# Optimization experiments

Measured on AMD Instinct MI355X. Metric: run time of the kernel, lower is better.

Reference implementation:

```python
import jax, jax.numpy as jnp
import numpy as np

B, L, D, H, FF, NS = 4, 1024, 1024, 16, 4096, 64
HD = D // H
EPS = 1e-5


def layer_norm(x, g, b):
    mu = jnp.mean(x, axis=-1, keepdims=True)
    var = jnp.mean(jnp.square(x - mu), axis=-1, keepdims=True)
    return (x - mu) * jax.lax.rsqrt(var + EPS) * g + b


def mha(xq, xkv, wqkv, bqkv, wo, bo, bias=None):
    # torch nn.MultiheadAttention with packed in_proj: rows [0:D]=Q, [D:2D]=K, [2D:3D]=V
    Bq, Lq, Dm = xq.shape
    q = (xq @ wqkv[:Dm].T + bqkv[:Dm]).reshape(Bq, Lq, H, HD).transpose(0, 2, 1, 3)
    k = (xkv @ wqkv[Dm:2 * Dm].T + bqkv[Dm:2 * Dm]).reshape(Bq, -1, H, HD).transpose(0, 2, 1, 3)
    v = (xkv @ wqkv[2 * Dm:].T + bqkv[2 * Dm:]).reshape(Bq, -1, H, HD).transpose(0, 2, 1, 3)
    scores = jnp.einsum('bhqd,bhkd->bhqk', q, k) / np.sqrt(HD).astype(np.float32)
    if bias is not None:
        scores = scores + bias.reshape(Bq, H, Lq, -1)
    attn = jax.nn.softmax(scores, axis=-1)
    out = jnp.einsum('bhqk,bhkd->bhqd', attn, v).transpose(0, 2, 1, 3).reshape(Bq, Lq, Dm)
    return out @ wo.T + bo


def setup_inputs() -> dict:
    key = jax.random.key(0)
    ks = jax.random.split(key, 16)
    w = lambda k, shape: jax.random.normal(k, shape, jnp.float32) * 0.02
    return {
        'x': jax.random.normal(ks[0], (B, L, D), jnp.float32),
        'alibi_bias': jax.random.normal(ks[1], (B * H, L, L), jnp.float32) * 0.1,
        'species_emb': jax.random.normal(ks[2], (B, NS, D), jnp.float32),
        'norm1_g': jnp.ones(D), 'norm1_b': jnp.zeros(D),
        'sa_wqkv': w(ks[3], (3 * D, D)), 'sa_bqkv': jnp.zeros(3 * D),
        'sa_wo': w(ks[4], (D, D)), 'sa_bo': jnp.zeros(D),
        'ca_nq_g': jnp.ones(D), 'ca_nq_b': jnp.zeros(D),
        'ca_nkv_g': jnp.ones(D), 'ca_nkv_b': jnp.zeros(D),
        'ca_wqkv': w(ks[5], (3 * D, D)), 'ca_bqkv': jnp.zeros(3 * D),
        'ca_wo': w(ks[6], (D, D)), 'ca_bo': jnp.zeros(D),
        'gate_param': jnp.float32(0.1),
        'ffn_g': jnp.ones(D), 'ffn_b': jnp.zeros(D),
        'ffn_w1': w(ks[7], (2 * FF, D)), 'ffn_b1': jnp.zeros(2 * FF),
        'ffn_w2': w(ks[8], (D, FF)), 'ffn_b2': jnp.zeros(D),
    }


def reference(x, alibi_bias, species_emb,
              norm1_g, norm1_b, sa_wqkv, sa_bqkv, sa_wo, sa_bo,
              ca_nq_g, ca_nq_b, ca_nkv_g, ca_nkv_b, ca_wqkv, ca_bqkv, ca_wo, ca_bo,
              gate_param, ffn_g, ffn_b, ffn_w1, ffn_b1, ffn_w2, ffn_b2):
    # 1) pre-norm self-attention with ALiBi additive bias
    h = layer_norm(x, norm1_g, norm1_b)
    h = mha(h, h, sa_wqkv, sa_bqkv, sa_wo, sa_bo, bias=alibi_bias)
    x = x + h  # dropout is identity in eval mode
    # 2) gated cross-attention with species embeddings
    q = layer_norm(x, ca_nq_g, ca_nq_b)
    kv = layer_norm(species_emb, ca_nkv_g, ca_nkv_b)
    cross = mha(q, kv, ca_wqkv, ca_bqkv, ca_wo, ca_bo)
    x = x + jax.nn.sigmoid(gate_param) * cross
    # 3) GEGLU feed-forward
    f = layer_norm(x, ffn_g, ffn_b) @ ffn_w1.T + ffn_b1
    val, gate = f[..., :FF], f[..., FF:]
    f = (val * jax.nn.gelu(gate, approximate=False)) @ ffn_w2.T + ffn_b2
    return x + f
```

## Files before the change

### kernel.cpp

```cpp
#include <hip/hip_runtime.h>
#include <hip/hip_bf16.h>
#include <cstdint>

#define DEVI __device__ __forceinline__

typedef __attribute__((ext_vector_type(8))) short  short8;
typedef __attribute__((ext_vector_type(8))) __bf16 bf16x8;
typedef __attribute__((ext_vector_type(4))) float  f32x4;

DEVI float bf2f(short s) {
    unsigned u = ((unsigned)(unsigned short)s) << 16;
    return __builtin_bit_cast(float, u);
}
DEVI short f2bf(float f) {
    unsigned u = __builtin_bit_cast(unsigned, f);
    u = u + 0x7FFF + ((u >> 16) & 1);
    return (short)(u >> 16);
}

__global__ __launch_bounds__(256) void cvt_bf16(const float* src, short* dst, long n) {
    const long i = ((long)blockIdx.x * 256 + threadIdx.x) * 8;
    const float4 a = *(const float4*)&src[i];
    const float4 b = *(const float4*)&src[i + 4];
    short8 o;
    o[0] = f2bf(a.x); o[1] = f2bf(a.y); o[2] = f2bf(a.z); o[3] = f2bf(a.w);
    o[4] = f2bf(b.x); o[5] = f2bf(b.y); o[6] = f2bf(b.z); o[7] = f2bf(b.w);
    *(short8*)&dst[i] = o;
}

struct GArgs {
    const short* A; long lda, sAb, sAh;
    const short* B; long ldb, sBb, sBh;
    short* C;       long ldc, sCb, sCh;
    const float* bias;
    const float* addm; long ldad, sDb, sDh;
    float* resid;
    float* outf;
    const float* gate;
    const float* addf;
    float scale;
    int K, nh;
};

template<int BM, int BN, int EPI>
__global__ __launch_bounds__(256) void gemm_bt(GArgs a) {
    constexpr int WM = BM / 2, WN = BN / 2, MI = WM / 16, NI = WN / 16;
    __shared__ __align__(16) short As[BM * 32];
    __shared__ __align__(16) short Bs[BN * 32];
    const int tid = threadIdx.x;
    const int wave = tid >> 6, lane = tid & 63;
    const int wm = (wave >> 1) * WM, wn = (wave & 1) * WN;
    const int q = lane >> 4, r = lane & 15;
    const int gx = gridDim.x, gy = gridDim.y;
    int flat = (int)(blockIdx.y * gx + blockIdx.x);
    { const int cp = (gx * gy) >> 3; flat = (flat & 7) * cp + (flat >> 3); }
    const int bx = flat % gx, by = flat / gx;
    const long bb = blockIdx.z / a.nh, hh = blockIdx.z % a.nh;
    const short* Ab = a.A + bb * a.sAb + hh * a.sAh + (long)by * BM * a.lda;
    const short* Bb = a.B + bb * a.sBb + hh * a.sBh + (long)bx * BN * a.ldb;
    const int trow = tid >> 2;
    const int tcol = (tid & 3) * 8;
    f32x4 acc[MI][NI] = {};

    for (int k0 = 0; k0 < a.K; k0 += 32) {
        __syncthreads();
#pragma unroll
        for (int i = 0; i < BM / 64; i++) {
            const short* g = Ab + (long)(i * 64 + trow) * a.lda + k0 + tcol;
            __builtin_amdgcn_global_load_lds(
                (const __attribute__((address_space(1))) void*)g,
                (__attribute__((address_space(3))) void*)&As[(i * 64 + trow) * 32 + tcol],
                16, 0, 0);
        }
#pragma unroll
        for (int i = 0; i < BN / 64; i++) {
            const short* g = Bb + (long)(i * 64 + trow) * a.ldb + k0 + tcol;
            __builtin_amdgcn_global_load_lds(
                (const __attribute__((address_space(1))) void*)g,
                (__attribute__((address_space(3))) void*)&Bs[(i * 64 + trow) * 32 + tcol],
                16, 0, 0);
        }
        asm volatile("s_waitcnt vmcnt(0)" ::: "memory");
        __syncthreads();
        bf16x8 av[MI], bv[NI];
#pragma unroll
        for (int mi = 0; mi < MI; mi++)
            av[mi] = __builtin_bit_cast(bf16x8, *(const short8*)&As[(wm + mi * 16 + r) * 32 + q * 8]);
#pragma unroll
        for (int ni = 0; ni < NI; ni++)
            bv[ni] = __builtin_bit_cast(bf16x8, *(const short8*)&Bs[(wn + ni * 16 + r) * 32 + q * 8]);
#pragma unroll
        for (int mi = 0; mi < MI; mi++)
#pragma unroll
            for (int ni = 0; ni < NI; ni++)
                acc[mi][ni] = __builtin_amdgcn_mfma_f32_16x16x32_bf16(av[mi], bv[ni], acc[mi][ni], 0, 0, 0);
    }

    const long m0 = (long)by * BM + wm;
    const long n0 = (long)bx * BN + wn;
    float gs = a.scale;
    if (EPI == 2 && a.gate) gs *= 1.f / (1.f + __expf(-(*a.gate)));
#pragma unroll
    for (int mi = 0; mi < MI; mi++)
#pragma unroll
        for (int ni = 0; ni < NI; ni++)
#pragma unroll
            for (int j = 0; j < 4; j++) {
                const long m = m0 + mi * 16 + q * 4 + j;
                const long n = n0 + ni * 16 + r;
                float v = acc[mi][ni][j];
                if constexpr (EPI == 0) {
                    if (a.bias) v += a.bias[n];
                    a.C[bb * a.sCb + hh * a.sCh + m * a.ldc + n] = f2bf(v);
                } else if constexpr (EPI == 1) {
                    v *= a.scale;
                    if (a.addm) v += a.addm[bb * a.sDb + hh * a.sDh + m * a.ldad + n];
                    a.C[bb * a.sCb + hh * a.sCh + m * a.ldc + n] = f2bf(v);
                } else if constexpr (EPI == 2) {
                    if (a.bias) v += a.bias[n];
                    const long idx = m * a.ldc + n;
                    const float base = a.addf ? a.addf[idx] : a.resid[idx];
                    a.resid[idx] = base + gs * v;
                } else {
                    if (a.bias) v += a.bias[n];
                    a.outf[m * a.ldc + n] = a.resid[m * a.ldc + n] + v;
                }
            }
}

struct GGArgs {
    const short* A; long lda;
    const short* Bv; const short* Bg; long ldb;
    short* C; long ldc;
    const float* b1;
    int K;
};
__global__ __launch_bounds__(256) void gemm_geglu(GGArgs a) {
    constexpr int BM = 128, BN = 64, WM = 64, WN = 32, MI = 4, NI = 2;
    __shared__ __align__(16) short As[BM * 32];
    __shared__ __align__(16) short Bs[BN * 32];
    __shared__ __align__(16) short Gs[BN * 32];
    const int tid = threadIdx.x;
    const int wave = tid >> 6, lane = tid & 63;
    const int wm = (wave >> 1) * WM, wn = (wave & 1) * WN;
    const int q = lane >> 4, r = lane & 15;
    const int gx = gridDim.x, gy = gridDim.y;
    int flat = (int)(blockIdx.y * gx + blockIdx.x);
    { const int cp = (gx * gy) >> 3; flat = (flat & 7) * cp + (flat >> 3); }
    const int bx = flat % gx, by = flat / gx;
    const short* Ab = a.A + (long)by * BM * a.lda;
    const short* Bb = a.Bv + (long)bx * BN * a.ldb;
    const short* Gb = a.Bg + (long)bx * BN * a.ldb;
    const int trow = tid >> 2, tcol = (tid & 3) * 8;
    f32x4 accv[MI][NI] = {}, accg[MI][NI] = {};

    for (int k0 = 0; k0 < a.K; k0 += 32) {
        __syncthreads();
#pragma unroll
        for (int i = 0; i < 2; i++) {
            const short* g = Ab + (long)(i * 64 + trow) * a.lda + k0 + tcol;
            __builtin_amdgcn_global_load_lds(
                (const __attribute__((address_space(1))) void*)g,
                (__attribute__((address_space(3))) void*)&As[(i * 64 + trow) * 32 + tcol],
                16, 0, 0);
        }
        {
            const short* g = Bb + (long)trow * a.ldb + k0 + tcol;
            __builtin_amdgcn_global_load_lds(
                (const __attribute__((address_space(1))) void*)g,
                (__attribute__((address_space(3))) void*)&Bs[trow * 32 + tcol], 16, 0, 0);
            const short* g2 = Gb + (long)trow * a.ldb + k0 + tcol;
            __builtin_amdgcn_global_load_lds(
                (const __attribute__((address_space(1))) void*)g2,
                (__attribute__((address_space(3))) void*)&Gs[trow * 32 + tcol], 16, 0, 0);
        }
        asm volatile("s_waitcnt vmcnt(0)" ::: "memory");
        __syncthreads();
        bf16x8 av[MI], bv[NI], gv[NI];
#pragma unroll
        for (int mi = 0; mi < MI; mi++)
            av[mi] = __builtin_bit_cast(bf16x8, *(const short8*)&As[(wm + mi * 16 + r) * 32 + q * 8]);
#pragma unroll
        for (int ni = 0; ni < NI; ni++) {
            bv[ni] = __builtin_bit_cast(bf16x8, *(const short8*)&Bs[(wn + ni * 16 + r) * 32 + q * 8]);
            gv[ni] = __builtin_bit_cast(bf16x8, *(const short8*)&Gs[(wn + ni * 16 + r) * 32 + q * 8]);
        }
#pragma unroll
        for (int mi = 0; mi < MI; mi++)
#pragma unroll
            for (int ni = 0; ni < NI; ni++) {
                accv[mi][ni] = __builtin_amdgcn_mfma_f32_16x16x32_bf16(av[mi], bv[ni], accv[mi][ni], 0, 0, 0);
                accg[mi][ni] = __builtin_amdgcn_mfma_f32_16x16x32_bf16(av[mi], gv[ni], accg[mi][ni], 0, 0, 0);
            }
    }

    const long m0 = (long)by * BM + wm;
    const long n0 = (long)bx * BN + wn;
#pragma unroll
    for (int mi = 0; mi < MI; mi++)
#pragma unroll
        for (int ni = 0; ni < NI; ni++)
#pragma unroll
            for (int j = 0; j < 4; j++) {
                const long m = m0 + mi * 16 + q * 4 + j;
                const long n = n0 + ni * 16 + r;
                const float v = accv[mi][ni][j] + a.b1[n];
                const float g = accg[mi][ni][j] + a.b1[4096 + n];
                const float ge = 0.5f * g * (1.f + erff(g * 0.7071067811865476f));
                a.C[m * a.ldc + n] = f2bf(v * ge);
            }
}

__global__ __launch_bounds__(256) void flash_sa(const short* qkv, const short* vt,
                                                const float* alibi, short* Obuf) {
    __shared__ __align__(16) short Qs[64 * 64], Ks[64 * 64], Vs[64 * 64], Ps[64 * 64];
    const int tid = threadIdx.x;
    const int wave = tid >> 6, lane = tid & 63, q = lane >> 4, r = lane & 15;
    int flat = (int)(blockIdx.y * 16 + blockIdx.x);
    flat = (flat & 7) * 128 + (flat >> 3);
    const int qt = flat & 15, bh = flat >> 4, b = bh >> 4, h = bh & 15;
    const long qrow0 = (long)b * 1024 + qt * 64;
    const int rw = tid >> 3, sp = tid & 7;

#pragma unroll
    for (int i = 0; i < 2; i++) {
        const int row = i * 32 + rw;
        const int c8 = (sp ^ (row & 7)) * 8;
        const short* g = qkv + (qrow0 + row) * 3072 + h * 64 + c8;
        __builtin_amdgcn_global_load_lds(
            (const __attribute__((address_space(1))) void*)g,
            (__attribute__((address_space(3))) void*)&Qs[row * 64 + sp * 8], 16, 0, 0);
    }

    f32x4 o[4] = {};
    float m_run[4], l_run[4];
#pragma unroll
    for (int j = 0; j < 4; j++) { m_run[j] = -1e30f; l_run[j] = 0.f; }

    for (int kt = 0; kt < 16; kt++) {
        __syncthreads();
#pragma unroll
        for (int i = 0; i < 2; i++) {
            const int row = i * 32 + rw;
            const int c8 = (sp ^ (row & 7)) * 8;
            const short* gk = qkv + ((long)b * 1024 + kt * 64 + row) * 3072 + 1024 + h * 64 + c8;
            __builtin_amdgcn_global_load_lds(
                (const __attribute__((address_space(1))) void*)gk,
                (__attribute__((address_space(3))) void*)&Ks[row * 64 + sp * 8], 16, 0, 0);
            const short* gv = vt + ((long)bh * 64 + row) * 1024 + kt * 64 + c8;
            __builtin_amdgcn_global_load_lds(
                (const __attribute__((address_space(1))) void*)gv,
                (__attribute__((address_space(3))) void*)&Vs[row * 64 + sp * 8], 16, 0, 0);
        }
        float al[4][4];
        const float* ab = alibi + (long)bh * 1048576 + (long)(qt * 64 + wave * 16) * 1024 + kt * 64;
#pragma unroll
        for (int ni = 0; ni < 4; ni++)
#pragma unroll
            for (int j = 0; j < 4; j++)
                al[ni][j] = ab[(q * 4 + j) * 1024 + ni * 16 + r];
        asm volatile("s_waitcnt vmcnt(0)" ::: "memory");
        __syncthreads();

        f32x4 sacc[4] = {};
        const int arow = wave * 16 + r;
#pragma unroll
        for (int kk = 0; kk < 2; kk++) {
            const bf16x8 av = __builtin_bit_cast(bf16x8,
                *(const short8*)&Qs[arow * 64 + (((kk * 4 + q) ^ (arow & 7)) * 8)]);
#pragma unroll
            for (int ni = 0; ni < 4; ni++) {
                const int brow = ni * 16 + r;
                const bf16x8 bv = __builtin_bit_cast(bf16x8,
                    *(const short8*)&Ks[brow * 64 + (((kk * 4 + q) ^ (brow & 7)) * 8)]);
                sacc[ni] = __builtin_amdgcn_mfma_f32_16x16x32_bf16(av, bv, sacc[ni], 0, 0, 0);
            }
        }
        float s[4][4];
#pragma unroll
        for (int ni = 0; ni < 4; ni++)
#pragma unroll
            for (int j = 0; j < 4; j++)
                s[ni][j] = sacc[ni][j] * 0.125f + al[ni][j];

        float p[4][4];
#pragma unroll
        for (int j = 0; j < 4; j++) {
            float mx = fmaxf(fmaxf(s[0][j], s[1][j]), fmaxf(s[2][j], s[3][j]));
#pragma unroll
            for (int off = 8; off; off >>= 1) mx = fmaxf(mx, __shfl_xor(mx, off));
            const float newm = fmaxf(m_run[j], mx);
            const float sc = __expf(m_run[j] - newm);
            m_run[j] = newm;
            float rs = 0.f;
#pragma unroll
            for (int ni = 0; ni < 4; ni++) { p[ni][j] = __expf(s[ni][j] - newm); rs += p[ni][j]; }
#pragma unroll
            for (int off = 8; off; off >>= 1) rs += __shfl_xor(rs, off);
            l_run[j] = l_run[j] * sc + rs;
#pragma unroll
            for (int nd = 0; nd < 4; nd++) o[nd][j] *= sc;
        }

#pragma unroll
        for (int ni = 0; ni < 4; ni++)
#pragma unroll
            for (int j = 0; j < 4; j++) {
                const int row = wave * 16 + q * 4 + j;
                const int col = ni * 16 + r;
                const int scol = (((col >> 3) ^ (row & 7)) << 3) | (col & 7);
                Ps[row * 64 + scol] = f2bf(p[ni][j]);
            }
        asm volatile("s_waitcnt lgkmcnt(0)" ::: "memory");

        const int prow = wave * 16 + r;
#pragma unroll
        for (int kk = 0; kk < 2; kk++) {
            const bf16x8 pa = __builtin_bit_cast(bf16x8,
                *(const short8*)&Ps[prow * 64 + (((kk * 4 + q) ^ (prow & 7)) * 8)]);
#pragma unroll
            for (int nd = 0; nd < 4; nd++) {
                const int vrow = nd * 16 + r;
                const bf16x8 vv = __builtin_bit_cast(bf16x8,
                    *(const short8*)&Vs[vrow * 64 + (((kk * 4 + q) ^ (vrow & 7)) * 8)]);
                o[nd] = __builtin_amdgcn_mfma_f32_16x16x32_bf16(pa, vv, o[nd], 0, 0, 0);
            }
        }
    }

#pragma unroll
    for (int nd = 0; nd < 4; nd++)
#pragma unroll
        for (int j = 0; j < 4; j++) {
            const long m = qrow0 + wave * 16 + q * 4 + j;
            Obuf[m * 1024 + h * 64 + nd * 16 + r] = f2bf(o[nd][j] / l_run[j]);
        }
}

__global__ __launch_bounds__(256) void flash_ca(const short* q2, const short* kv2,
                                                const short* vt, short* Obuf) {
    __shared__ __align__(16) short Qs[64 * 64], Ks[64 * 64], Vs[64 * 64], Ps[64 * 64];
    const int tid = threadIdx.x;
    const int wave = tid >> 6, lane = tid & 63, q = lane >> 4, r = lane & 15;
    int flat = (int)(blockIdx.y * 16 + blockIdx.x);
    flat = (flat & 7) * 128 + (flat >> 3);
    const int qt = flat & 15, bh = flat >> 4, b = bh >> 4, h = bh & 15;
    const long qrow0 = (long)b * 1024 + qt * 64;
    const int rw = tid >> 3, sp = tid & 7;

#pragma unroll
    for (int i = 0; i < 2; i++) {
        const int row = i * 32 + rw;
        const int c8 = (sp ^ (row & 7)) * 8;
        const short* gq = q2 + (qrow0 + row) * 1024 + h * 64 + c8;
        __builtin_amdgcn_global_load_lds(
            (const __attribute__((address_space(1))) void*)gq,
            (__attribute__((address_space(3))) void*)&Qs[row * 64 + sp * 8], 16, 0, 0);
        const short* gk = kv2 + ((long)b * 64 + row) * 2048 + h * 64 + c8;
        __builtin_amdgcn_global_load_lds(
            (const __attribute__((address_space(1))) void*)gk,
            (__attribute__((address_space(3))) void*)&Ks[row * 64 + sp * 8], 16, 0, 0);
        const short* gv = vt + ((long)bh * 64 + row) * 64 + c8;
        __builtin_amdgcn_global_load_lds(
            (const __attribute__((address_space(1))) void*)gv,
            (__attribute__((address_space(3))) void*)&Vs[row * 64 + sp * 8], 16, 0, 0);
    }
    asm volatile("s_waitcnt vmcnt(0)" ::: "memory");
    __syncthreads();

    f32x4 sacc[4] = {};
    const int arow = wave * 16 + r;
#pragma unroll
    for (int kk = 0; kk < 2; kk++) {
        const bf16x8 av = __builtin_bit_cast(bf16x8,
            *(const short8*)&Qs[arow * 64 + (((kk * 4 + q) ^ (arow & 7)) * 8)]);
#pragma unroll
        for (int ni = 0; ni < 4; ni++) {
            const int brow = ni * 16 + r;
            const bf16x8 bv = __builtin_bit_cast(bf16x8,
                *(const short8*)&Ks[brow * 64 + (((kk * 4 + q) ^ (brow & 7)) * 8)]);
            sacc[ni] = __builtin_amdgcn_mfma_f32_16x16x32_bf16(av, bv, sacc[ni], 0, 0, 0);
        }
    }
    float p[4][4], linv[4];
#pragma unroll
    for (int j = 0; j < 4; j++) {
        float s0 = sacc[0][j] * 0.125f, s1 = sacc[1][j] * 0.125f;
        float s2 = sacc[2][j] * 0.125f, s3 = sacc[3][j] * 0.125f;
        float mx = fmaxf(fmaxf(s0, s1), fmaxf(s2, s3));
#pragma unroll
        for (int off = 8; off; off >>= 1) mx = fmaxf(mx, __shfl_xor(mx, off));
        p[0][j] = __expf(s0 - mx); p[1][j] = __expf(s1 - mx);
        p[2][j] = __expf(s2 - mx); p[3][j] = __expf(s3 - mx);
        float rs = p[0][j] + p[1][j] + p[2][j] + p[3][j];
#pragma unroll
        for (int off = 8; off; off >>= 1) rs += __shfl_xor(rs, off);
        linv[j] = 1.f / rs;
    }
#pragma unroll
    for (int ni = 0; ni < 4; ni++)
#pragma unroll
        for (int j = 0; j < 4; j++) {
            const int row = wave * 16 + q * 4 + j;
            const int col = ni * 16 + r;
            const int scol = (((col >> 3) ^ (row & 7)) << 3) | (col & 7);
            Ps[row * 64 + scol] = f2bf(p[ni][j]);
        }
    asm volatile("s_waitcnt lgkmcnt(0)" ::: "memory");

    f32x4 o[4] = {};
    const int prow = wave * 16 + r;
#pragma unroll
    for (int kk = 0; kk < 2; kk++) {
        const bf16x8 pa = __builtin_bit_cast(bf16x8,
            *(const short8*)&Ps[prow * 64 + (((kk * 4 + q) ^ (prow & 7)) * 8)]);
#pragma unroll
        for (int nd = 0; nd < 4; nd++) {
            const int vrow = nd * 16 + r;
            const bf16x8 vv = __builtin_bit_cast(bf16x8,
                *(const short8*)&Vs[vrow * 64 + (((kk * 4 + q) ^ (vrow & 7)) * 8)]);
            o[nd] = __builtin_amdgcn_mfma_f32_16x16x32_bf16(pa, vv, o[nd], 0, 0, 0);
        }
    }
#pragma unroll
    for (int nd = 0; nd < 4; nd++)
#pragma unroll
        for (int j = 0; j < 4; j++) {
            const long m = qrow0 + wave * 16 + q * 4 + j;
            Obuf[m * 1024 + h * 64 + nd * 16 + r] = f2bf(o[nd][j] * linv[j]);
        }
}

__global__ __launch_bounds__(256) void ln_rows(const float* X, const float* gw,
                                               const float* bw, short* Y) {
    const long row = blockIdx.x;
    const float* x = X + row * 1024;
    const int t = threadIdx.x;
    float v[4], s1 = 0.f, s2 = 0.f;
#pragma unroll
    for (int i = 0; i < 4; i++) {
        v[i] = x[t + i * 256];
        s1 += v[i]; s2 += v[i] * v[i];
    }
#pragma unroll
    for (int o = 32; o; o >>= 1) { s1 += __shfl_xor(s1, o); s2 += __shfl_xor(s2, o); }
    __shared__ float sm[8];
    if ((t & 63) == 0) { sm[t >> 6] = s1; sm[4 + (t >> 6)] = s2; }
    __syncthreads();
    s1 = sm[0] + sm[1] + sm[2] + sm[3];
    s2 = sm[4] + sm[5] + sm[6] + sm[7];
    const float mu = s1 * (1.f / 1024.f);
    const float var = s2 * (1.f / 1024.f) - mu * mu;
    const float rr = rsqrtf(var + 1e-5f);
#pragma unroll
    for (int i = 0; i < 4; i++) {
        const int c = t + i * 256;
        Y[row * 1024 + c] = f2bf((v[i] - mu) * rr * gw[c] + bw[c]);
    }
}

__global__ __launch_bounds__(256) void softmax1024(short* S) {
    const long row = blockIdx.x;
    short* p = S + row * 1024;
    const int t = threadIdx.x;
    float v[4];
#pragma unroll
    for (int i = 0; i < 4; i++) v[i] = bf2f(p[t + i * 256]);
    float m = fmaxf(fmaxf(v[0], v[1]), fmaxf(v[2], v[3]));
#pragma unroll
    for (int o = 32; o; o >>= 1) m = fmaxf(m, __shfl_xor(m, o));
    __shared__ float sm[4];
    if ((t & 63) == 0) sm[t >> 6] = m;
    __syncthreads();
    m = fmaxf(fmaxf(sm[0], sm[1]), fmaxf(sm[2], sm[3]));
    float e[4], s = 0.f;
#pragma unroll
    for (int i = 0; i < 4; i++) { e[i] = __expf(v[i] - m); s += e[i]; }
#pragma unroll
    for (int o = 32; o; o >>= 1) s += __shfl_xor(s, o);
    __syncthreads();
    if ((t & 63) == 0) sm[t >> 6] = s;
    __syncthreads();
    s = sm[0] + sm[1] + sm[2] + sm[3];
    const float inv = 1.f / s;
#pragma unroll
    for (int i = 0; i < 4; i++) p[t + i * 256] = f2bf(e[i] * inv);
}

__global__ __launch_bounds__(256) void softmax64(short* S) {
    const long row = (long)blockIdx.x * 4 + (threadIdx.x >> 6);
    const int lane = threadIdx.x & 63;
    short* p = S + row * 64;
    float v = bf2f(p[lane]);
    float m = v;
#pragma unroll
    for (int o = 32; o; o >>= 1) m = fmaxf(m, __shfl_xor(m, o));
    float e = __expf(v - m), s = e;
#pragma unroll
    for (int o = 32; o; o >>= 1) s += __shfl_xor(s, o);
    p[lane] = f2bf(e / s);
}

__global__ __launch_bounds__(256) void transpose_v_sa(const short* qkv, short* vt) {
    __shared__ short tbuf[64][68];
    const int j0 = blockIdx.x * 64, h = blockIdx.y, b = blockIdx.z;
    const int tid = threadIdx.x;
#pragma unroll
    for (int i = 0; i < 16; i++) {
        const int idx = i * 256 + tid, jj = idx >> 6, hd = idx & 63;
        tbuf[jj][hd] = qkv[(long)(b * 1024 + j0 + jj) * 3072 + 2048 + h * 64 + hd];
    }
    __syncthreads();
    const long bh = b * 16 + h;
#pragma unroll
    for (int i = 0; i < 16; i++) {
        const int idx = i * 256 + tid, hd = idx >> 6, jj = idx & 63;
        vt[(bh * 64 + hd) * 1024 + j0 + jj] = tbuf[jj][hd];
    }
}

__global__ __launch_bounds__(256) void transpose_v_ca(const short* kv2, short* vt2) {
    __shared__ short tbuf[64][68];
    const int bh = blockIdx.x, b = bh >> 4, h = bh & 15;
    const int tid = threadIdx.x;
#pragma unroll
    for (int i = 0; i < 16; i++) {
        const int idx = i * 256 + tid, jj = idx >> 6, hd = idx & 63;
        tbuf[jj][hd] = kv2[(long)(b * 64 + jj) * 2048 + 1024 + h * 64 + hd];
    }
    __syncthreads();
#pragma unroll
    for (int i = 0; i < 16; i++) {
        const int idx = i * 256 + tid, hd = idx >> 6, jj = idx & 63;
        vt2[((long)bh * 64 + hd) * 64 + jj] = tbuf[jj][hd];
    }
}

__global__ __launch_bounds__(256) void geglu_inplace(short* f1) {
    const long i = (long)blockIdx.x * 256 + threadIdx.x;
    const long m = i >> 9, j8 = (i & 511) * 8;
    const short8 av = *(const short8*)&f1[m * 8192 + j8];
    const short8 gv = *(const short8*)&f1[m * 8192 + 4096 + j8];
    short8 o;
#pragma unroll
    for (int jj = 0; jj < 8; jj++) {
        const float xv = bf2f(av[jj]), gg = bf2f(gv[jj]);
        const float ge = 0.5f * gg * (1.f + erff(gg * 0.7071067811865476f));
        o[jj] = f2bf(xv * ge);
    }
    *(short8*)&f1[m * 8192 + j8] = o;
}

extern "C" void kernel_launch(void* const* d_in, const int* in_sizes, int n_in,
                              void* d_out, int out_size, void* d_ws, size_t ws_size,
                              hipStream_t stream) {
    const float* x        = (const float*)d_in[0];
    const float* alibi    = (const float*)d_in[1];
    const float* species  = (const float*)d_in[2];
    const float* n1g      = (const float*)d_in[3];
    const float* n1b      = (const float*)d_in[4];
    const float* sa_wqkv  = (const float*)d_in[5];
    const float* sa_bqkv  = (const float*)d_in[6];
    const float* sa_wo    = (const float*)d_in[7];
    const float* sa_bo    = (const float*)d_in[8];
    const float* ca_nq_g  = (const float*)d_in[9];
    const float* ca_nq_b  = (const float*)d_in[10];
    const float* ca_nkv_g = (const float*)d_in[11];
    const float* ca_nkv_b = (const float*)d_in[12];
    const float* ca_wqkv  = (const float*)d_in[13];
    const float* ca_bqkv  = (const float*)d_in[14];
    const float* ca_wo    = (const float*)d_in[15];
    const float* ca_bo    = (const float*)d_in[16];
    const float* gate     = (const float*)d_in[17];
    const float* ffn_g    = (const float*)d_in[18];
    const float* ffn_b    = (const float*)d_in[19];
    const float* ffn_w1   = (const float*)d_in[20];
    const float* ffn_b1   = (const float*)d_in[21];
    const float* ffn_w2   = (const float*)d_in[22];
    const float* ffn_b2   = (const float*)d_in[23];
    float* out = (float*)d_out;

    const dim3 blk(256);
    char* ws = (char*)d_ws;

    if (ws_size >= (304ull << 20)) {
        float* resid  = (float*)(ws);
        short* lnbuf  = (short*)(ws + (16l << 20));
        short* Obuf   = (short*)(ws + (24l << 20));
        short* vt     = (short*)(ws + (32l << 20));
        short* qkv    = (short*)(ws + (40l << 20));
        short* w_saq  = (short*)(ws + (64l << 20));
        short* w_sawo = (short*)(ws + (70l << 20));
        short* w_caq  = (short*)(ws + (72l << 20));
        short* w_cawo = (short*)(ws + (78l << 20));
        short* w_f1   = (short*)(ws + (80l << 20));
        short* w_f2   = (short*)(ws + (96l << 20));
        short* kv2    = (short*)(ws + (104l << 20));
        short* g1     = (short*)(ws + (240l << 20));

        cvt_bf16<<<1536, blk, 0, stream>>>(sa_wqkv, w_saq, 3145728);
        cvt_bf16<<<512,  blk, 0, stream>>>(sa_wo,   w_sawo, 1048576);
        cvt_bf16<<<1536, blk, 0, stream>>>(ca_wqkv, w_caq, 3145728);
        cvt_bf16<<<512,  blk, 0, stream>>>(ca_wo,   w_cawo, 1048576);
        cvt_bf16<<<4096, blk, 0, stream>>>(ffn_w1,  w_f1, 8388608);
        cvt_bf16<<<2048, blk, 0, stream>>>(ffn_w2,  w_f2, 4194304);

        ln_rows<<<4096, blk, 0, stream>>>(x, n1g, n1b, lnbuf);

        {
            GArgs a{}; a.A = lnbuf; a.lda = 1024; a.B = w_saq; a.ldb = 1024;
            a.C = qkv; a.ldc = 3072; a.bias = sa_bqkv; a.K = 1024; a.nh = 1; a.scale = 1.f;
            gemm_bt<128, 128, 0><<<dim3(24, 32, 1), blk, 0, stream>>>(a);
        }
        transpose_v_sa<<<dim3(16, 16, 4), blk, 0, stream>>>(qkv, vt);

        flash_sa<<<dim3(16, 64), blk, 0, stream>>>(qkv, vt, alibi, Obuf);

        {
            GArgs a{}; a.A = Obuf; a.lda = 1024; a.B = w_sawo; a.ldb = 1024;
            a.ldc = 1024; a.bias = sa_bo; a.resid = resid; a.addf = x;
            a.scale = 1.f; a.K = 1024; a.nh = 1;
            gemm_bt<128, 64, 2><<<dim3(16, 32, 1), blk, 0, stream>>>(a);
        }

        ln_rows<<<4096, blk, 0, stream>>>(resid, ca_nq_g, ca_nq_b, lnbuf);
        {
            GArgs a{}; a.A = lnbuf; a.lda = 1024; a.B = w_caq; a.ldb = 1024;
            a.C = qkv; a.ldc = 1024; a.bias = ca_bqkv; a.K = 1024; a.nh = 1; a.scale = 1.f;
            gemm_bt<128, 64, 0><<<dim3(16, 32, 1), blk, 0, stream>>>(a);
        }
        ln_rows<<<256, blk, 0, stream>>>(species, ca_nkv_g, ca_nkv_b, lnbuf);
        {
            GArgs a{}; a.A = lnbuf; a.lda = 1024; a.B = w_caq + 1024 * 1024; a.ldb = 1024;
            a.C = kv2; a.ldc = 2048; a.bias = ca_bqkv + 1024; a.K = 1024; a.nh = 1; a.scale = 1.f;
            gemm_bt<128, 128, 0><<<dim3(16, 2, 1), blk, 0, stream>>>(a);
        }
        transpose_v_ca<<<64, blk, 0, stream>>>(kv2, vt);

        flash_ca<<<dim3(16, 64), blk, 0, stream>>>(qkv, kv2, vt, Obuf);

        {
            GArgs a{}; a.A = Obuf; a.lda = 1024; a.B = w_cawo; a.ldb = 1024;
            a.ldc = 1024; a.bias = ca_bo; a.resid = resid; a.gate = gate;
            a.scale = 1.f; a.K = 1024; a.nh = 1;
            gemm_bt<128, 64, 2><<<dim3(16, 32, 1), blk, 0, stream>>>(a);
        }

        ln_rows<<<4096, blk, 0, stream>>>(resid, ffn_g, ffn_b, lnbuf);
        {
            GGArgs a{}; a.A = lnbuf; a.lda = 1024;
            a.Bv = w_f1; a.Bg = w_f1 + (long)4096 * 1024; a.ldb = 1024;
            a.C = g1; a.ldc = 4096; a.b1 = ffn_b1; a.K = 1024;
            gemm_geglu<<<dim3(64, 32, 1), blk, 0, stream>>>(a);
        }
        {
            GArgs a{}; a.A = g1; a.lda = 4096; a.B = w_f2; a.ldb = 4096;
            a.ldc = 1024; a.bias = ffn_b2; a.resid = resid; a.outf = out;
            a.scale = 1.f; a.K = 4096; a.nh = 1;
            gemm_bt<128, 64, 3><<<dim3(16, 32, 1), blk, 0, stream>>>(a);
        }
        return;
    }

    float* resid  = (float*)(ws);
    short* lnbuf  = (short*)(ws + (16l << 20));
    short* Obuf   = (short*)(ws + (24l << 20));
    short* vt     = (short*)(ws + (32l << 20));
    short* qkv    = (short*)(ws + (40l << 20));
    short* Sbuf   = (short*)(ws + (64l << 20));
    short* f1     = Sbuf;
    short* kv2    = qkv + 4194304;
    short* w_sawo = (short*)(ws + (80l << 20));
    short* w_caq  = (short*)(ws + (82l << 20));
    short* w_cawo = (short*)(ws + (88l << 20));
    short* w_saq  = (short*)(ws + (90l << 20));
    short* w_f1   = qkv;
    short* w_f2   = (short*)(ws + (56l << 20));

    cvt_bf16<<<1536, blk, 0, stream>>>(sa_wqkv, w_saq, 3145728);
    cvt_bf16<<<512,  blk, 0, stream>>>(sa_wo,   w_sawo, 1048576);
    cvt_bf16<<<1536, blk, 0, stream>>>(ca_wqkv, w_caq, 3145728);
    cvt_bf16<<<512,  blk, 0, stream>>>(ca_wo,   w_cawo, 1048576);

    hipMemcpyAsync(resid, x, (size_t)4194304 * 4, hipMemcpyDeviceToDevice, stream);
    ln_rows<<<4096, blk, 0, stream>>>(x, n1g, n1b, lnbuf);

    {
        GArgs a{}; a.A = lnbuf; a.lda = 1024; a.B = w_saq; a.ldb = 1024;
        a.C = qkv; a.ldc = 3072; a.bias = sa_bqkv; a.K = 1024; a.nh = 1; a.scale = 1.f;
        gemm_bt<128, 128, 0><<<dim3(24, 32, 1), blk, 0, stream>>>(a);
    }
    transpose_v_sa<<<dim3(16, 16, 4), blk, 0, stream>>>(qkv, vt);

    for (int c = 0; c < 8; c++) {
        const int b = c >> 1, hc = c & 1;
        const long boff = (long)b * 1024 * 3072;
        {
            GArgs a{}; a.A = qkv + boff + hc * 512; a.lda = 3072; a.sAh = 64;
            a.B = qkv + boff + 1024 + hc * 512; a.ldb = 3072; a.sBh = 64;
            a.C = Sbuf; a.ldc = 1024; a.sCh = 1048576;
            a.addm = alibi + ((long)(b * 16 + hc * 8)) * 1048576; a.ldad = 1024; a.sDh = 1048576;
            a.scale = 0.125f; a.K = 64; a.nh = 8;
            gemm_bt<128, 128, 1><<<dim3(8, 8, 8), blk, 0, stream>>>(a);
        }
        softmax1024<<<8192, blk, 0, stream>>>(Sbuf);
        {
            GArgs a{}; a.A = Sbuf; a.lda = 1024; a.sAh = 1048576;
            a.B = vt + (long)b * 1048576 + (long)hc * 8 * 65536; a.ldb = 1024; a.sBh = 65536;
            a.C = Obuf + (long)b * 1048576 + hc * 512; a.ldc = 1024; a.sCh = 64;
            a.K = 1024; a.nh = 8; a.scale = 1.f;
            gemm_bt<64, 64, 0><<<dim3(1, 16, 8), blk, 0, stream>>>(a);
        }
    }
    {
        GArgs a{}; a.A = Obuf; a.lda = 1024; a.B = w_sawo; a.ldb = 1024;
        a.ldc = 1024; a.bias = sa_bo; a.resid = resid; a.scale = 1.f; a.K = 1024; a.nh = 1;
        gemm_bt<128, 128, 2><<<dim3(8, 32, 1), blk, 0, stream>>>(a);
    }

    ln_rows<<<4096, blk, 0, stream>>>(resid, ca_nq_g, ca_nq_b, lnbuf);
    {
        GArgs a{}; a.A = lnbuf; a.lda = 1024; a.B = w_caq; a.ldb = 1024;
        a.C = qkv; a.ldc = 1024; a.bias = ca_bqkv; a.K = 1024; a.nh = 1; a.scale = 1.f;
        gemm_bt<128, 128, 0><<<dim3(8, 32, 1), blk, 0, stream>>>(a);
    }
    ln_rows<<<256, blk, 0, stream>>>(species, ca_nkv_g, ca_nkv_b, lnbuf);
    {
        GArgs a{}; a.A = lnbuf; a.lda = 1024; a.B = w_caq + 1024 * 1024; a.ldb = 1024;
        a.C = kv2; a.ldc = 2048; a.bias = ca_bqkv + 1024; a.K = 1024; a.nh = 1; a.scale = 1.f;
        gemm_bt<128, 128, 0><<<dim3(16, 2, 1), blk, 0, stream>>>(a);
    }
    transpose_v_ca<<<64, blk, 0, stream>>>(kv2, vt);
    {
        GArgs a{}; a.A = qkv; a.lda = 1024; a.sAb = 1048576; a.sAh = 64;
        a.B = kv2; a.ldb = 2048; a.sBb = 131072; a.sBh = 64;
        a.C = Sbuf; a.ldc = 64; a.sCb = 1048576; a.sCh = 65536;
        a.scale = 0.125f; a.K = 64; a.nh = 16;
        gemm_bt<64, 64, 1><<<dim3(1, 16, 64), blk, 0, stream>>>(a);
    }
    cvt_bf16<<<4096, blk, 0, stream>>>(ffn_w1, w_f1, 8388608);
    cvt_bf16<<<2048, blk, 0, stream>>>(ffn_w2, w_f2, 4194304);

    softmax64<<<16384, blk, 0, stream>>>(Sbuf);
    {
        GArgs a{}; a.A = Sbuf; a.lda = 64; a.sAb = 1048576; a.sAh = 65536;
        a.B = vt; a.ldb = 64; a.sBb = 65536; a.sBh = 4096;
        a.C = Obuf; a.ldc = 1024; a.sCb = 1048576; a.sCh = 64;
        a.K = 64; a.nh = 16; a.scale = 1.f;
        gemm_bt<64, 64, 0><<<dim3(1, 16, 64), blk, 0, stream>>>(a);
    }
    {
        GArgs a{}; a.A = Obuf; a.lda = 1024; a.B = w_cawo; a.ldb = 1024;
        a.ldc = 1024; a.bias = ca_bo; a.resid = resid; a.gate = gate;
        a.scale = 1.f; a.K = 1024; a.nh = 1;
        gemm_bt<128, 128, 2><<<dim3(8, 32, 1), blk, 0, stream>>>(a);
    }

    ln_rows<<<4096, blk, 0, stream>>>(resid, ffn_g, ffn_b, lnbuf);
    for (int rc = 0; rc < 2; rc++) {
        const long ro = (long)rc * 2048;
        {
            GArgs a{}; a.A = lnbuf + ro * 1024; a.lda = 1024; a.B = w_f1; a.ldb = 1024;
            a.C = f1; a.ldc = 8192; a.bias = ffn_b1; a.K = 1024; a.nh = 1; a.scale = 1.f;
            gemm_bt<128, 128, 0><<<dim3(64, 16, 1), blk, 0, stream>>>(a);
        }
        geglu_inplace<<<4096, blk, 0, stream>>>(f1);
        {
            GArgs a{}; a.A = f1; a.lda = 8192; a.B = w_f2; a.ldb = 4096;
            a.ldc = 1024; a.bias = ffn_b2; a.resid = resid + ro * 1024; a.outf = out + ro * 1024;
            a.scale = 1.f; a.K = 4096; a.nh = 1;
            gemm_bt<128, 128, 3><<<dim3(8, 16, 1), blk, 0, stream>>>(a);
        }
    }
}
```

Before: 928.9 us.

## Double-buffer LDS tiles in GEMMs and flash attention, fuse weight conversions

Adds two LDS buffers to the GEMM, GEGLU GEMM and self-attention flash kernels so the next K tile is prefetched with global_load_lds while MFMAs run on the current one. Each iteration now ends with one barrier instead of two. Flash attention holds Q in registers, reuses the P buffer to stage Q, and prefetches K/V for the next tile. The six weight-conversion launches are merged into one kernel. The extra LDS per block may lower occupancy, and the wait at the end of each iteration still drains all outstanding loads.

```diff
diff --git a/kernel.cpp b/kernel.cpp
--- a/kernel.cpp
+++ b/kernel.cpp
@@ -17,6 +17,10 @@
     u = u + 0x7FFF + ((u >> 16) & 1);
     return (short)(u >> 16);
 }
+
+#define GLDS(gp, lp) __builtin_amdgcn_global_load_lds( \
+    (const __attribute__((address_space(1))) void*)(gp), \
+    (__attribute__((address_space(3))) void*)(lp), 16, 0, 0)
 
 __global__ __launch_bounds__(256) void cvt_bf16(const float* src, short* dst, long n) {
     const long i = ((long)blockIdx.x * 256 + threadIdx.x) * 8;
@@ -26,6 +30,22 @@
     o[0] = f2bf(a.x); o[1] = f2bf(a.y); o[2] = f2bf(a.z); o[3] = f2bf(a.w);
     o[4] = f2bf(b.x); o[5] = f2bf(b.y); o[6] = f2bf(b.z); o[7] = f2bf(b.w);
     *(short8*)&dst[i] = o;
+}
+
+struct CvtArgs {
+    const float* src[6]; short* dst[6]; int blkStart[7];
+};
+__global__ __launch_bounds__(256) void cvt_all(CvtArgs c) {
+    const int b = blockIdx.x;
+    int s = 0;
+    while (b >= c.blkStart[s + 1]) s++;
+    const long i = ((long)(b - c.blkStart[s]) * 256 + threadIdx.x) * 8;
+    const float4 a0 = *(const float4*)&c.src[s][i];
+    const float4 a1 = *(const float4*)&c.src[s][i + 4];
+    short8 o;
+    o[0] = f2bf(a0.x); o[1] = f2bf(a0.y); o[2] = f2bf(a0.z); o[3] = f2bf(a0.w);
+    o[4] = f2bf(a1.x); o[5] = f2bf(a1.y); o[6] = f2bf(a1.z); o[7] = f2bf(a1.w);
+    *(short8*)&c.dst[s][i] = o;
 }
 
 struct GArgs {
@@ -45,8 +65,8 @@
 template<int BM, int BN, int EPI>
 __global__ __launch_bounds__(256) void gemm_bt(GArgs a) {
     constexpr int WM = BM / 2, WN = BN / 2, MI = WM / 16, NI = WN / 16;
-    __shared__ __align__(16) short As[BM * 32];
-    __shared__ __align__(16) short Bs[BN * 32];
+    __shared__ __align__(16) short As[2][BM * 32];
+    __shared__ __align__(16) short Bs[2][BN * 32];
     const int tid = threadIdx.x;
     const int wave = tid >> 6, lane = tid & 63;
     const int wm = (wave >> 1) * WM, wn = (wave & 1) * WN;
@@ -61,39 +81,41 @@
     const int trow = tid >> 2;
     const int tcol = (tid & 3) * 8;
     f32x4 acc[MI][NI] = {};
-
-    for (int k0 = 0; k0 < a.K; k0 += 32) {
-        __syncthreads();
-#pragma unroll
-        for (int i = 0; i < BM / 64; i++) {
-            const short* g = Ab + (long)(i * 64 + trow) * a.lda + k0 + tcol;
-            __builtin_amdgcn_global_load_lds(
-                (const __attribute__((address_space(1))) void*)g,
-                (__attribute__((address_space(3))) void*)&As[(i * 64 + trow) * 32 + tcol],
-                16, 0, 0);
-        }
-#pragma unroll
-        for (int i = 0; i < BN / 64; i++) {
-            const short* g = Bb + (long)(i * 64 + trow) * a.ldb + k0 + tcol;
-            __builtin_amdgcn_global_load_lds(
-                (const __attribute__((address_space(1))) void*)g,
-                (__attribute__((address_space(3))) void*)&Bs[(i * 64 + trow) * 32 + tcol],
-                16, 0, 0);
-        }
-        asm volatile("s_waitcnt vmcnt(0)" ::: "memory");
-        __syncthreads();
+    const int nt = a.K >> 5;
+
+    auto stage = [&](int buf, int k0) {
+#pragma unroll
+        for (int i = 0; i < BM / 64; i++)
+            GLDS(Ab + (long)(i * 64 + trow) * a.lda + k0 + tcol,
+                 &As[buf][(i * 64 + trow) * 32 + tcol]);
+#pragma unroll
+        for (int i = 0; i < BN / 64; i++)
+            GLDS(Bb + (long)(i * 64 + trow) * a.ldb + k0 + tcol,
+                 &Bs[buf][(i * 64 + trow) * 32 + tcol]);
+    };
+
+    stage(0, 0);
+    asm volatile("s_waitcnt vmcnt(0)" ::: "memory");
+    __builtin_amdgcn_s_barrier();
+
+    int cur = 0;
+    for (int t = 0; t < nt; ++t) {
+        if (t + 1 < nt) stage(cur ^ 1, (t + 1) << 5);
         bf16x8 av[MI], bv[NI];
 #pragma unroll
         for (int mi = 0; mi < MI; mi++)
-            av[mi] = __builtin_bit_cast(bf16x8, *(const short8*)&As[(wm + mi * 16 + r) * 32 + q * 8]);
+            av[mi] = __builtin_bit_cast(bf16x8, *(const short8*)&As[cur][(wm + mi * 16 + r) * 32 + q * 8]);
 #pragma unroll
         for (int ni = 0; ni < NI; ni++)
-            bv[ni] = __builtin_bit_cast(bf16x8, *(const short8*)&Bs[(wn + ni * 16 + r) * 32 + q * 8]);
+            bv[ni] = __builtin_bit_cast(bf16x8, *(const short8*)&Bs[cur][(wn + ni * 16 + r) * 32 + q * 8]);
 #pragma unroll
         for (int mi = 0; mi < MI; mi++)
 #pragma unroll
             for (int ni = 0; ni < NI; ni++)
                 acc[mi][ni] = __builtin_amdgcn_mfma_f32_16x16x32_bf16(av[mi], bv[ni], acc[mi][ni], 0, 0, 0);
+        asm volatile("s_waitcnt vmcnt(0) lgkmcnt(0)" ::: "memory");
+        __builtin_amdgcn_s_barrier();
+        cur ^= 1;
     }
 
     const long m0 = (long)by * BM + wm;
@@ -137,9 +159,9 @@
 };
 __global__ __launch_bounds__(256) void gemm_geglu(GGArgs a) {
     constexpr int BM = 128, BN = 64, WM = 64, WN = 32, MI = 4, NI = 2;
-    __shared__ __align__(16) short As[BM * 32];
-    __shared__ __align__(16) short Bs[BN * 32];
-    __shared__ __align__(16) short Gs[BN * 32];
+    __shared__ __align__(16) short As[2][BM * 32];
+    __shared__ __align__(16) short Bs[2][BN * 32];
+    __shared__ __align__(16) short Gs[2][BN * 32];
     const int tid = threadIdx.x;
     const int wave = tid >> 6, lane = tid & 63;
     const int wm = (wave >> 1) * WM, wn = (wave & 1) * WN;
@@ -153,37 +175,32 @@
     const short* Gb = a.Bg + (long)bx * BN * a.ldb;
     const int trow = tid >> 2, tcol = (tid & 3) * 8;
     f32x4 accv[MI][NI] = {}, accg[MI][NI] = {};
-
-    for (int k0 = 0; k0 < a.K; k0 += 32) {
-        __syncthreads();
-#pragma unroll
-        for (int i = 0; i < 2; i++) {
-            const short* g = Ab + (long)(i * 64 + trow) * a.lda + k0 + tcol;
-            __builtin_amdgcn_global_load_lds(
-                (const __attribute__((address_space(1))) void*)g,
-                (__attribute__((address_space(3))) void*)&As[(i * 64 + trow) * 32 + tcol],
-                16, 0, 0);
-        }
-        {
-            const short* g = Bb + (long)trow * a.ldb + k0 + tcol;
-            __builtin_amdgcn_global_load_lds(
-                (const __attribute__((address_space(1))) void*)g,
-                (__attribute__((address_space(3))) void*)&Bs[trow * 32 + tcol], 16, 0, 0);
-            const short* g2 = Gb + (long)trow * a.ldb + k0 + tcol;
-            __builtin_amdgcn_global_load_lds(
-                (const __attribute__((address_space(1))) void*)g2,
-                (__attribute__((address_space(3))) void*)&Gs[trow * 32 + tcol], 16, 0, 0);
-        }
-        asm volatile("s_waitcnt vmcnt(0)" ::: "memory");
-        __syncthreads();
+    const int nt = a.K >> 5;
+
+    auto stage = [&](int buf, int k0) {
+#pragma unroll
+        for (int i = 0; i < 2; i++)
+            GLDS(Ab + (long)(i * 64 + trow) * a.lda + k0 + tcol,
+                 &As[buf][(i * 64 + trow) * 32 + tcol]);
+        GLDS(Bb + (long)trow * a.ldb + k0 + tcol, &Bs[buf][trow * 32 + tcol]);
+        GLDS(Gb + (long)trow * a.ldb + k0 + tcol, &Gs[buf][trow * 32 + tcol]);
+    };
+
+    stage(0, 0);
+    asm volatile("s_waitcnt vmcnt(0)" ::: "memory");
+    __builtin_amdgcn_s_barrier();
+
+    int cur = 0;
+    for (int t = 0; t < nt; ++t) {
+        if (t + 1 < nt) stage(cur ^ 1, (t + 1) << 5);
         bf16x8 av[MI], bv[NI], gv[NI];
 #pragma unroll
         for (int mi = 0; mi < MI; mi++)
-            av[mi] = __builtin_bit_cast(bf16x8, *(const short8*)&As[(wm + mi * 16 + r) * 32 + q * 8]);
+            av[mi] = __builtin_bit_cast(bf16x8, *(const short8*)&As[cur][(wm + mi * 16 + r) * 32 + q * 8]);
 #pragma unroll
         for (int ni = 0; ni < NI; ni++) {
-            bv[ni] = __builtin_bit_cast(bf16x8, *(const short8*)&Bs[(wn + ni * 16 + r) * 32 + q * 8]);
-            gv[ni] = __builtin_bit_cast(bf16x8, *(const short8*)&Gs[(wn + ni * 16 + r) * 32 + q * 8]);
+            bv[ni] = __builtin_bit_cast(bf16x8, *(const short8*)&Bs[cur][(wn + ni * 16 + r) * 32 + q * 8]);
+            gv[ni] = __builtin_bit_cast(bf16x8, *(const short8*)&Gs[cur][(wn + ni * 16 + r) * 32 + q * 8]);
         }
 #pragma unroll
         for (int mi = 0; mi < MI; mi++)
@@ -192,6 +209,9 @@
                 accv[mi][ni] = __builtin_amdgcn_mfma_f32_16x16x32_bf16(av[mi], bv[ni], accv[mi][ni], 0, 0, 0);
                 accg[mi][ni] = __builtin_amdgcn_mfma_f32_16x16x32_bf16(av[mi], gv[ni], accg[mi][ni], 0, 0, 0);
             }
+        asm volatile("s_waitcnt vmcnt(0) lgkmcnt(0)" ::: "memory");
+        __builtin_amdgcn_s_barrier();
+        cur ^= 1;
     }
 
     const long m0 = (long)by * BM + wm;
@@ -213,7 +233,8 @@
 
 __global__ __launch_bounds__(256) void flash_sa(const short* qkv, const short* vt,
                                                 const float* alibi, short* Obuf) {
-    __shared__ __align__(16) short Qs[64 * 64], Ks[64 * 64], Vs[64 * 64], Ps[64 * 64];
+    __shared__ __align__(16) short Ps[64 * 64];
+    __shared__ __align__(16) short Ks[2][64 * 64], Vs[2][64 * 64];
     const int tid = threadIdx.x;
     const int wave = tid >> 6, lane = tid & 63, q = lane >> 4, r = lane & 15;
     int flat = (int)(blockIdx.y * 16 + blockIdx.x);
@@ -222,36 +243,42 @@
     const long qrow0 = (long)b * 1024 + qt * 64;
     const int rw = tid >> 3, sp = tid & 7;
 
+    auto stage_kv = [&](int buf, int kt) {
+#pragma unroll
+        for (int i = 0; i < 2; i++) {
+            const int row = i * 32 + rw;
+            const int c8 = (sp ^ (row & 7)) * 8;
+            GLDS(qkv + ((long)b * 1024 + kt * 64 + row) * 3072 + 1024 + h * 64 + c8,
+                 &Ks[buf][row * 64 + sp * 8]);
+            GLDS(vt + ((long)bh * 64 + row) * 1024 + kt * 64 + c8,
+                 &Vs[buf][row * 64 + sp * 8]);
+        }
+    };
+
 #pragma unroll
     for (int i = 0; i < 2; i++) {
         const int row = i * 32 + rw;
         const int c8 = (sp ^ (row & 7)) * 8;
-        const short* g = qkv + (qrow0 + row) * 3072 + h * 64 + c8;
-        __builtin_amdgcn_global_load_lds(
-            (const __attribute__((address_space(1))) void*)g,
-            (__attribute__((address_space(3))) void*)&Qs[row * 64 + sp * 8], 16, 0, 0);
-    }
+        GLDS(qkv + (qrow0 + row) * 3072 + h * 64 + c8, &Ps[row * 64 + sp * 8]);
+    }
+    stage_kv(0, 0);
+    asm volatile("s_waitcnt vmcnt(0)" ::: "memory");
+    __builtin_amdgcn_s_barrier();
+
+    const int arow = wave * 16 + r;
+    bf16x8 qv[2];
+#pragma unroll
+    for (int kk = 0; kk < 2; kk++)
+        qv[kk] = __builtin_bit_cast(bf16x8,
+            *(const short8*)&Ps[arow * 64 + (((kk * 4 + q) ^ (arow & 7)) * 8)]);
 
     f32x4 o[4] = {};
     float m_run[4], l_run[4];
 #pragma unroll
     for (int j = 0; j < 4; j++) { m_run[j] = -1e30f; l_run[j] = 0.f; }
 
+    int cur = 0;
     for (int kt = 0; kt < 16; kt++) {
-        __syncthreads();
-#pragma unroll
-        for (int i = 0; i < 2; i++) {
-            const int row = i * 32 + rw;
-            const int c8 = (sp ^ (row & 7)) * 8;
-            const short* gk = qkv + ((long)b * 1024 + kt * 64 + row) * 3072 + 1024 + h * 64 + c8;
-            __builtin_amdgcn_global_load_lds(
-                (const __attribute__((address_space(1))) void*)gk,
-                (__attribute__((address_space(3))) void*)&Ks[row * 64 + sp * 8], 16, 0, 0);
-            const short* gv = vt + ((long)bh * 64 + row) * 1024 + kt * 64 + c8;
-            __builtin_amdgcn_global_load_lds(
-                (const __attribute__((address_space(1))) void*)gv,
-                (__attribute__((address_space(3))) void*)&Vs[row * 64 + sp * 8], 16, 0, 0);
-        }
         float al[4][4];
         const float* ab = alibi + (long)bh * 1048576 + (long)(qt * 64 + wave * 16) * 1024 + kt * 64;
 #pragma unroll
@@ -259,21 +286,17 @@
 #pragma unroll
             for (int j = 0; j < 4; j++)
                 al[ni][j] = ab[(q * 4 + j) * 1024 + ni * 16 + r];
-        asm volatile("s_waitcnt vmcnt(0)" ::: "memory");
-        __syncthreads();
+        if (kt < 15) stage_kv(cur ^ 1, kt + 1);
 
         f32x4 sacc[4] = {};
-        const int arow = wave * 16 + r;
 #pragma unroll
         for (int kk = 0; kk < 2; kk++) {
-            const bf16x8 av = __builtin_bit_cast(bf16x8,
-                *(const short8*)&Qs[arow * 64 + (((kk * 4 + q) ^ (arow & 7)) * 8)]);
 #pragma unroll
             for (int ni = 0; ni < 4; ni++) {
                 const int brow = ni * 16 + r;
                 const bf16x8 bv = __builtin_bit_cast(bf16x8,
-                    *(const short8*)&Ks[brow * 64 + (((kk * 4 + q) ^ (brow & 7)) * 8)]);
-                sacc[ni] = __builtin_amdgcn_mfma_f32_16x16x32_bf16(av, bv, sacc[ni], 0, 0, 0);
+                    *(const short8*)&Ks[cur][brow * 64 + (((kk * 4 + q) ^ (brow & 7)) * 8)]);
+                sacc[ni] = __builtin_amdgcn_mfma_f32_16x16x32_bf16(qv[kk], bv, sacc[ni], 0, 0, 0);
             }
         }
         float s[4][4];
@@ -322,10 +345,13 @@
             for (int nd = 0; nd < 4; nd++) {
                 const int vrow = nd * 16 + r;
                 const bf16x8 vv = __builtin_bit_cast(bf16x8,
-                    *(const short8*)&Vs[vrow * 64 + (((kk * 4 + q) ^ (vrow & 7)) * 8)]);
+                    *(const short8*)&Vs[cur][vrow * 64 + (((kk * 4 + q) ^ (vrow & 7)) * 8)]);
                 o[nd] = __builtin_amdgcn_mfma_f32_16x16x32_bf16(pa, vv, o[nd], 0, 0, 0);
             }
         }
+        asm volatile("s_waitcnt vmcnt(0) lgkmcnt(0)" ::: "memory");
+        __builtin_amdgcn_s_barrier();
+        cur ^= 1;
     }
 
 #pragma unroll
@@ -352,18 +378,9 @@
     for (int i = 0; i < 2; i++) {
         const int row = i * 32 + rw;
         const int c8 = (sp ^ (row & 7)) * 8;
-        const short* gq = q2 + (qrow0 + row) * 1024 + h * 64 + c8;
-        __builtin_amdgcn_global_load_lds(
-            (const __attribute__((address_space(1))) void*)gq,
-            (__attribute__((address_space(3))) void*)&Qs[row * 64 + sp * 8], 16, 0, 0);
-        const short* gk = kv2 + ((long)b * 64 + row) * 2048 + h * 64 + c8;
-        __builtin_amdgcn_global_load_lds(
-            (const __attribute__((address_space(1))) void*)gk,
-            (__attribute__((address_space(3))) void*)&Ks[row * 64 + sp * 8], 16, 0, 0);
-        const short* gv = vt + ((long)bh * 64 + row) * 64 + c8;
-        __builtin_amdgcn_global_load_lds(
-            (const __attribute__((address_space(1))) void*)gv,
-            (__attribute__((address_space(3))) void*)&Vs[row * 64 + sp * 8], 16, 0, 0);
+        GLDS(q2 + (qrow0 + row) * 1024 + h * 64 + c8, &Qs[row * 64 + sp * 8]);
+        GLDS(kv2 + ((long)b * 64 + row) * 2048 + h * 64 + c8, &Ks[row * 64 + sp * 8]);
+        GLDS(vt + ((long)bh * 64 + row) * 64 + c8, &Vs[row * 64 + sp * 8]);
     }
     asm volatile("s_waitcnt vmcnt(0)" ::: "memory");
     __syncthreads();
@@ -598,12 +615,20 @@
         short* kv2    = (short*)(ws + (104l << 20));
         short* g1     = (short*)(ws + (240l << 20));
 
-        cvt_bf16<<<1536, blk, 0, stream>>>(sa_wqkv, w_saq, 3145728);
-        cvt_bf16<<<512,  blk, 0, stream>>>(sa_wo,   w_sawo, 1048576);
-        cvt_bf16<<<1536, blk, 0, stream>>>(ca_wqkv, w_caq, 3145728);
-        cvt_bf16<<<512,  blk, 0, stream>>>(ca_wo,   w_cawo, 1048576);
-        cvt_bf16<<<4096, blk, 0, stream>>>(ffn_w1,  w_f1, 8388608);
-        cvt_bf16<<<2048, blk, 0, stream>>>(ffn_w2,  w_f2, 4194304);
+        {
+            CvtArgs c{};
+            c.src[0] = sa_wqkv; c.dst[0] = w_saq;
+            c.src[1] = sa_wo;   c.dst[1] = w_sawo;
+            c.src[2] = ca_wqkv; c.dst[2] = w_caq;
+            c.src[3] = ca_wo;   c.dst[3] = w_cawo;
+            c.src[4] = ffn_w1;  c.dst[4] = w_f1;
+            c.src[5] = ffn_w2;  c.dst[5] = w_f2;
+            const int nb[6] = {1536, 512, 1536, 512, 4096, 2048};
+            int acc = 0;
+            for (int i = 0; i < 6; i++) { c.blkStart[i] = acc; acc += nb[i]; }
+            c.blkStart[6] = acc;
+            cvt_all<<<acc, blk, 0, stream>>>(c);
+        }
 
         ln_rows<<<4096, blk, 0, stream>>>(x, n1g, n1b, lnbuf);
 
```

After: 910.5 us. 1.02x faster.
